# Performance work log

Hardware: AMD Instinct MI355X
Metric: run time of the kernel (lower is better)

## Reference

```python
import jax, jax.numpy as jnp
import numpy as np

H = 512  # hidden_size


def setup_inputs() -> dict:
    key = jax.random.key(0)
    k1, k2, k3, k4, k5, k6 = jax.random.split(key, 6)
    B, S = 32, 2048
    output = jax.random.normal(k1, (B, H), dtype=jnp.float32)
    encoder_outputs = jax.random.normal(k2, (B, S, 2 * H), dtype=jnp.float32)
    encoder_mask = jax.random.randint(k3, (B, S), 0, 2, dtype=jnp.int32)
    # nn.Linear(3H, H): weight [H, 3H], bias [H]
    bound = 1.0 / np.sqrt(3 * H)
    W_attn = jax.random.uniform(k4, (H, 3 * H), minval=-bound, maxval=bound, dtype=jnp.float32)
    b_attn = jax.random.uniform(k5, (H,), minval=-bound, maxval=bound, dtype=jnp.float32)
    v = jax.random.normal(k6, (H,), dtype=jnp.float32) * (1.0 / np.sqrt(H))
    return {"output": output, "encoder_outputs": encoder_outputs,
            "encoder_mask": encoder_mask, "W_attn": W_attn, "b_attn": b_attn, "v": v}


def reference(output, encoder_outputs, encoder_mask, W_attn, b_attn, v):
    # Equivalent to cat([repeat(output), enc], -1) @ W.T: split W into state/enc blocks
    W_s = W_attn[:, :H]        # [H, H]   acts on decoder state
    W_e = W_attn[:, H:]        # [H, 2H]  acts on encoder outputs
    state_proj = output @ W_s.T                              # [B, H]
    enc_proj = jnp.einsum('bse,he->bsh', encoder_outputs, W_e)  # [B, S, H]
    energy = jnp.tanh(state_proj[:, None, :] + enc_proj + b_attn)  # [B, S, H]
    scores = jnp.einsum('bsh,h->bs', energy, v)[:, None, :]   # [B, 1, S]
    scores = scores - 1000.0 * (encoder_mask[:, None, :] == 0).astype(scores.dtype)
    return jax.nn.softmax(scores, axis=2)
```

## Files before the change

### kernel.cpp

```cpp
#include <hip/hip_runtime.h>
#include <hip/hip_bf16.h>

typedef __attribute__((ext_vector_type(4))) float f32x4;
typedef __attribute__((ext_vector_type(8))) short short8;

#define HH 512
#define BB 32
#define SS 2048
#define KK 1024

__device__ __forceinline__ unsigned short f2bf(float f) {
    unsigned int u = __float_as_uint(f);
    u += 0x7fffu + ((u >> 16) & 1u);
    return (unsigned short)(u >> 16);
}

__device__ __forceinline__ ushort4 pack4(float4 f) {
    ushort4 p;
    p.x = f2bf(f.x); p.y = f2bf(f.y); p.z = f2bf(f.z); p.w = f2bf(f.w);
    return p;
}

__device__ __forceinline__ float fast_tanh(float x) {
    float e = __expf(2.0f * x);
    return 1.0f - 2.0f / (e + 1.0f);
}

__device__ __forceinline__ void async_copy16(const void* g, void* l) {
    __builtin_amdgcn_global_load_lds(
        (__attribute__((address_space(1))) const void*)g,
        (__attribute__((address_space(3))) void*)l, 16, 0, 0);
}

__global__ __launch_bounds__(256)
void spb_kernel(const float* __restrict__ out_state,
                const float* __restrict__ W,
                const float* __restrict__ bias,
                float* __restrict__ spb) {
    int wave = threadIdx.x >> 6, lane = threadIdx.x & 63;
    int g = blockIdx.x * 4 + wave;
    int b = g >> 9, h = g & 511;
    const float* wr = W + (size_t)h * 1536;
    const float* ov = out_state + b * HH;
    float4 w0 = *(const float4*)(wr + lane * 8);
    float4 w1 = *(const float4*)(wr + lane * 8 + 4);
    float4 o0 = *(const float4*)(ov + lane * 8);
    float4 o1 = *(const float4*)(ov + lane * 8 + 4);
    float d = w0.x * o0.x + w0.y * o0.y + w0.z * o0.z + w0.w * o0.w
            + w1.x * o1.x + w1.y * o1.y + w1.z * o1.z + w1.w * o1.w;
    d += __shfl_xor(d, 1); d += __shfl_xor(d, 2); d += __shfl_xor(d, 4);
    d += __shfl_xor(d, 8); d += __shfl_xor(d, 16); d += __shfl_xor(d, 32);
    if (lane == 0) spb[g] = d + bias[h];
}

__global__ void wconv_kernel(const float* __restrict__ W, unsigned short* __restrict__ Wt) {
    int idx = blockIdx.x * 256 + threadIdx.x;
    int e8 = idx * 8;
    int h = e8 >> 10;
    int k = e8 & 1023;
    const float* src = W + (size_t)h * 1536 + 512 + k;
    float4 w0 = *(const float4*)src;
    float4 w1 = *(const float4*)(src + 4);
    int kt = k >> 5;
    int q  = (k >> 3) & 3;
    int g  = h >> 4;
    int r  = h & 15;
    int ln = (q << 4) | r;
    unsigned short* dst = Wt + (size_t)kt * 16384 + g * 512 + ln * 8;
    *(ushort4*)dst = pack4(w0);
    *(ushort4*)(dst + 4) = pack4(w1);
}

__global__ __launch_bounds__(512, 4)
void attn_gemm(const float* __restrict__ enc, const unsigned short* __restrict__ Wt,
               const float* __restrict__ spb, const float* __restrict__ vvec,
               float* __restrict__ scores) {
    __shared__ __align__(16) unsigned short Asm[2][2048];
    __shared__ __align__(16) unsigned short Bsm[2][16384];
    __shared__ float red[8][64];

    const int tid = threadIdx.x;
    const int w = tid >> 6;
    const int lane = tid & 63;
    const int r = lane & 15;
    const int q = lane >> 4;
    const int b = blockIdx.x >> 5;
    const int s0 = (blockIdx.x & 31) << 6;

    const int arow = tid >> 3;
    const int akq  = tid & 7;
    const float* asrc = enc + ((size_t)(b * SS + s0 + arow)) * KK + akq * 4;
    const int akey = (arow ^ (arow >> 2)) & 3;
    const int ast  = arow * 32 + ((((akq >> 1) ^ akey) << 3) | ((akq & 1) << 2));

    const unsigned short* bsrc = Wt + tid * 8;

    const int rkey = (r ^ (r >> 2)) & 3;
    const int ard  = r * 32 + ((q ^ rkey) << 3);
    const int brd  = (w * 4) * 512 + lane * 8;

    f32x4 acc[4][4] = {};

    {
        float4 f0 = *(const float4*)asrc;
        #pragma unroll
        for (int c = 0; c < 4; ++c)
            async_copy16(bsrc + c * 4096, &Bsm[0][c * 4096 + tid * 8]);
        *(ushort4*)&Asm[0][ast] = pack4(f0);
    }
    __syncthreads();

    for (int p = 0; p < 32; ++p) {
        const int buf = p & 1;
        float4 f;
        if (p < 31) {
            f = *(const float4*)(asrc + (p + 1) * 32);
            const unsigned short* src = bsrc + (size_t)(p + 1) * 16384;
            #pragma unroll
            for (int c = 0; c < 4; ++c)
                async_copy16(src + c * 4096, &Bsm[buf ^ 1][c * 4096 + tid * 8]);
        }
        short8 af[4], bf[4];
        #pragma unroll
        for (int mt = 0; mt < 4; ++mt)
            af[mt] = *(const short8*)&Asm[buf][mt * 512 + ard];
        #pragma unroll
        for (int nf = 0; nf < 4; ++nf)
            bf[nf] = *(const short8*)&Bsm[buf][nf * 512 + brd];
        #pragma unroll
        for (int mt = 0; mt < 4; ++mt)
            #pragma unroll
            for (int nf = 0; nf < 4; ++nf)
                acc[mt][nf] = __builtin_amdgcn_mfma_f32_16x16x32_bf16(
                    af[mt], bf[nf], acc[mt][nf], 0, 0, 0);
        if (p < 31)
            *(ushort4*)&Asm[buf ^ 1][ast] = pack4(f);
        __syncthreads();
    }

    float vh[4], sh[4];
    #pragma unroll
    for (int nf = 0; nf < 4; ++nf) {
        int h = w * 64 + nf * 16 + r;
        vh[nf] = vvec[h];
        sh[nf] = spb[b * HH + h];
    }
    float rowacc[4][4] = {};
    #pragma unroll
    for (int mt = 0; mt < 4; ++mt)
        #pragma unroll
        for (int nf = 0; nf < 4; ++nf)
            #pragma unroll
            for (int i = 0; i < 4; ++i) {
                float x = acc[mt][nf][i] + sh[nf];
                rowacc[mt][i] += vh[nf] * fast_tanh(x);
            }
    #pragma unroll
    for (int mt = 0; mt < 4; ++mt)
        #pragma unroll
        for (int i = 0; i < 4; ++i) {
            float t = rowacc[mt][i];
            t += __shfl_xor(t, 1);
            t += __shfl_xor(t, 2);
            t += __shfl_xor(t, 4);
            t += __shfl_xor(t, 8);
            rowacc[mt][i] = t;
        }
    if (r == 0) {
        #pragma unroll
        for (int mt = 0; mt < 4; ++mt)
            #pragma unroll
            for (int i = 0; i < 4; ++i)
                red[w][mt * 16 + q * 4 + i] = rowacc[mt][i];
    }
    __syncthreads();
    if (tid < 64) {
        float sum = 0.f;
        #pragma unroll
        for (int ww = 0; ww < 8; ++ww) sum += red[ww][tid];
        scores[b * SS + s0 + tid] = sum;
    }
}

__global__ void softmax_kernel(const float* __restrict__ scores,
                               const int* __restrict__ mask,
                               float* __restrict__ out) {
    __shared__ float red[256];
    int b = blockIdx.x, tid = threadIdx.x;
    float x[8];
    #pragma unroll
    for (int i = 0; i < 8; ++i) {
        int s = tid + i * 256;
        float sc = scores[b * SS + s];
        if (mask[b * SS + s] == 0) sc -= 1000.0f;
        x[i] = sc;
    }
    float mx = x[0];
    #pragma unroll
    for (int i = 1; i < 8; ++i) mx = fmaxf(mx, x[i]);
    red[tid] = mx;
    __syncthreads();
    for (int o = 128; o > 0; o >>= 1) {
        if (tid < o) red[tid] = fmaxf(red[tid], red[tid + o]);
        __syncthreads();
    }
    mx = red[0];
    __syncthreads();
    float e[8], sum = 0.f;
    #pragma unroll
    for (int i = 0; i < 8; ++i) { e[i] = __expf(x[i] - mx); sum += e[i]; }
    red[tid] = sum;
    __syncthreads();
    for (int o = 128; o > 0; o >>= 1) {
        if (tid < o) red[tid] += red[tid + o];
        __syncthreads();
    }
    float inv = 1.0f / red[0];
    #pragma unroll
    for (int i = 0; i < 8; ++i) out[b * SS + tid + i * 256] = e[i] * inv;
}

extern "C" void kernel_launch(void* const* d_in, const int* in_sizes, int n_in,
                              void* d_out, int out_size, void* d_ws, size_t ws_size,
                              hipStream_t stream) {
    const float* out_state = (const float*)d_in[0];
    const float* enc       = (const float*)d_in[1];
    const int*   mask      = (const int*)d_in[2];
    const float* W_attn    = (const float*)d_in[3];
    const float* b_attn    = (const float*)d_in[4];
    const float* vvec      = (const float*)d_in[5];
    float* out = (float*)d_out;

    char* ws = (char*)d_ws;
    float*          spb    = (float*)ws;
    unsigned short* Wt     = (unsigned short*)(ws + 65536);
    float*          scores = (float*)(ws + 65536 + 1048576);

    spb_kernel<<<4096, 256, 0, stream>>>(out_state, W_attn, b_attn, spb);
    wconv_kernel<<<256, 256, 0, stream>>>(W_attn, Wt);
    attn_gemm<<<1024, 512, 0, stream>>>(enc, Wt, spb, vvec, scores);
    softmax_kernel<<<32, 256, 0, stream>>>(scores, mask, out);
}
```

Measured before the change: 445.6 us.

## Deepen A-tile prefetch and use explicit waitcnt barriers in attention GEMM

The encoder-tile global load is now issued two K-steps ahead and held in a register, so it stays in flight across a barrier. The plain __syncthreads is replaced by an explicit s_waitcnt vmcnt(1) plus s_barrier, which waits only for the LDS async copies and leaves the newest load pending. The last two iterations are peeled out of the loop. Each block also rotates the order of its weight-chunk copies by block index, to spread simultaneous accesses across memory channels. The aim is to hide global-memory latency in a loop that looks latency-bound. The cost is more register pressure and hand-written wait counts that depend on the compiler keeping the memory-op order.

```diff
diff --git a/kernel.cpp b/kernel.cpp
--- a/kernel.cpp
+++ b/kernel.cpp
@@ -84,8 +84,9 @@
     const int lane = tid & 63;
     const int r = lane & 15;
     const int q = lane >> 4;
-    const int b = blockIdx.x >> 5;
-    const int s0 = (blockIdx.x & 31) << 6;
+    const int bx = blockIdx.x;
+    const int b = bx >> 5;
+    const int s0 = (bx & 31) << 6;
 
     const int arow = tid >> 3;
     const int akq  = tid & 7;
@@ -101,25 +102,31 @@
 
     f32x4 acc[4][4] = {};
 
-    {
-        float4 f0 = *(const float4*)asrc;
-        #pragma unroll
-        for (int c = 0; c < 4; ++c)
-            async_copy16(bsrc + c * 4096, &Bsm[0][c * 4096 + tid * 8]);
-        *(ushort4*)&Asm[0][ast] = pack4(f0);
-    }
-    __syncthreads();
-
-    for (int p = 0; p < 32; ++p) {
+    #pragma unroll
+    for (int c = 0; c < 4; ++c) {
+        int cc = (c + bx) & 3;
+        async_copy16(bsrc + cc * 4096, &Bsm[0][cc * 4096 + tid * 8]);
+    }
+    asm volatile("" ::: "memory");
+    float4 f0 = *(const float4*)asrc;
+    float4 fcur = *(const float4*)(asrc + 32);
+    asm volatile("" ::: "memory");
+    *(ushort4*)&Asm[0][ast] = pack4(f0);
+    asm volatile("s_waitcnt vmcnt(1) lgkmcnt(0)" ::: "memory");
+    __builtin_amdgcn_s_barrier();
+
+    for (int p = 0; p < 30; ++p) {
         const int buf = p & 1;
-        float4 f;
-        if (p < 31) {
-            f = *(const float4*)(asrc + (p + 1) * 32);
-            const unsigned short* src = bsrc + (size_t)(p + 1) * 16384;
-            #pragma unroll
-            for (int c = 0; c < 4; ++c)
-                async_copy16(src + c * 4096, &Bsm[buf ^ 1][c * 4096 + tid * 8]);
+        #pragma unroll
+        for (int c = 0; c < 4; ++c) {
+            int cc = (c + bx) & 3;
+            async_copy16(bsrc + (size_t)(p + 1) * 16384 + cc * 4096,
+                         &Bsm[buf ^ 1][cc * 4096 + tid * 8]);
         }
+        asm volatile("" ::: "memory");
+        float4 fnext = *(const float4*)(asrc + (size_t)(p + 2) * 32);
+        asm volatile("" ::: "memory");
+
         short8 af[4], bf[4];
         #pragma unroll
         for (int mt = 0; mt < 4; ++mt)
@@ -133,9 +140,53 @@
             for (int nf = 0; nf < 4; ++nf)
                 acc[mt][nf] = __builtin_amdgcn_mfma_f32_16x16x32_bf16(
                     af[mt], bf[nf], acc[mt][nf], 0, 0, 0);
-        if (p < 31)
-            *(ushort4*)&Asm[buf ^ 1][ast] = pack4(f);
-        __syncthreads();
+
+        *(ushort4*)&Asm[buf ^ 1][ast] = pack4(fcur);
+        asm volatile("s_waitcnt vmcnt(1) lgkmcnt(0)" ::: "memory");
+        __builtin_amdgcn_s_barrier();
+        fcur = fnext;
+    }
+
+    {
+        #pragma unroll
+        for (int c = 0; c < 4; ++c) {
+            int cc = (c + bx) & 3;
+            async_copy16(bsrc + (size_t)31 * 16384 + cc * 4096,
+                         &Bsm[1][cc * 4096 + tid * 8]);
+        }
+        asm volatile("" ::: "memory");
+        short8 af[4], bf[4];
+        #pragma unroll
+        for (int mt = 0; mt < 4; ++mt)
+            af[mt] = *(const short8*)&Asm[0][mt * 512 + ard];
+        #pragma unroll
+        for (int nf = 0; nf < 4; ++nf)
+            bf[nf] = *(const short8*)&Bsm[0][nf * 512 + brd];
+        #pragma unroll
+        for (int mt = 0; mt < 4; ++mt)
+            #pragma unroll
+            for (int nf = 0; nf < 4; ++nf)
+                acc[mt][nf] = __builtin_amdgcn_mfma_f32_16x16x32_bf16(
+                    af[mt], bf[nf], acc[mt][nf], 0, 0, 0);
+        *(ushort4*)&Asm[1][ast] = pack4(fcur);
+        asm volatile("s_waitcnt vmcnt(0) lgkmcnt(0)" ::: "memory");
+        __builtin_amdgcn_s_barrier();
+    }
+
+    {
+        short8 af[4], bf[4];
+        #pragma unroll
+        for (int mt = 0; mt < 4; ++mt)
+            af[mt] = *(const short8*)&Asm[1][mt * 512 + ard];
+        #pragma unroll
+        for (int nf = 0; nf < 4; ++nf)
+            bf[nf] = *(const short8*)&Bsm[1][nf * 512 + brd];
+        #pragma unroll
+        for (int mt = 0; mt < 4; ++mt)
+            #pragma unroll
+            for (int nf = 0; nf < 4; ++nf)
+                acc[mt][nf] = __builtin_amdgcn_mfma_f32_16x16x32_bf16(
+                    af[mt], bf[nf], acc[mt][nf], 0, 0, 0);
     }
 
     float vh[4], sh[4];
```

New measurement: 432.1 us. -3.0%, faster.

## Stream fp32 encoder tiles via LDS DMA, convert in-register, read B fragments from global

Applied to the files above, without the earlier changes.

Restructures the attention GEMM so each block covers 128 sequence rows instead of 64. Encoder tiles are copied to LDS as fp32 via global_load_lds with an XOR swizzle and converted to bf16 in registers just before the MFMA. Weight fragments now load straight from global memory into registers, double-buffered, instead of being staged through LDS. Hand-placed waitcnt and barriers pipeline a 128-wide K chunk per stage. This is meant to cut VGPR-staged conversion stores and B-tile LDS traffic and to reuse B across more rows, at the cost of lower occupancy (2 blocks per SM) and 128KB of LDS, plus repeated conversion work.

```diff
diff --git a/kernel.cpp b/kernel.cpp
--- a/kernel.cpp
+++ b/kernel.cpp
@@ -26,10 +26,25 @@
     return 1.0f - 2.0f / (e + 1.0f);
 }
 
-__device__ __forceinline__ void async_copy16(const void* g, void* l) {
+__device__ __forceinline__ void dma16(const float* g, float* l) {
     __builtin_amdgcn_global_load_lds(
         (__attribute__((address_space(1))) const void*)g,
         (__attribute__((address_space(3))) void*)l, 16, 0, 0);
+}
+
+#define FENCE() asm volatile("" ::: "memory")
+
+__device__ __forceinline__ short8 cvt_bf8(f32x4 a0, f32x4 a1) {
+    short8 o;
+    #pragma unroll
+    for (int i = 0; i < 4; ++i) {
+        union { __hip_bfloat16 h; unsigned short u; } c0, c1;
+        c0.h = __float2bfloat16(a0[i]);
+        c1.h = __float2bfloat16(a1[i]);
+        o[i]     = (short)c0.u;
+        o[i + 4] = (short)c1.u;
+    }
+    return o;
 }
 
 __global__ __launch_bounds__(256)
@@ -71,73 +86,122 @@
     *(ushort4*)(dst + 4) = pack4(w1);
 }
 
-__global__ __launch_bounds__(512, 4)
+__global__ __launch_bounds__(512, 2)
 void attn_gemm(const float* __restrict__ enc, const unsigned short* __restrict__ Wt,
                const float* __restrict__ spb, const float* __restrict__ vvec,
                float* __restrict__ scores) {
-    __shared__ __align__(16) unsigned short Asm[2][2048];
-    __shared__ __align__(16) unsigned short Bsm[2][16384];
-    __shared__ float red[8][64];
+    __shared__ __align__(16) float Asm[2][16384];
 
     const int tid = threadIdx.x;
     const int w = tid >> 6;
     const int lane = tid & 63;
     const int r = lane & 15;
     const int q = lane >> 4;
-    const int b = blockIdx.x >> 5;
-    const int s0 = (blockIdx.x & 31) << 6;
-
-    const int arow = tid >> 3;
-    const int akq  = tid & 7;
-    const float* asrc = enc + ((size_t)(b * SS + s0 + arow)) * KK + akq * 4;
-    const int akey = (arow ^ (arow >> 2)) & 3;
-    const int ast  = arow * 32 + ((((akq >> 1) ^ akey) << 3) | ((akq & 1) << 2));
-
-    const unsigned short* bsrc = Wt + tid * 8;
-
-    const int rkey = (r ^ (r >> 2)) & 3;
-    const int ard  = r * 32 + ((q ^ rkey) << 3);
-    const int brd  = (w * 4) * 512 + lane * 8;
-
-    f32x4 acc[4][4] = {};
+    const int b = blockIdx.x >> 4;
+    const int s0 = (blockIdx.x & 15) << 7;
+    const int bS = b * SS + s0;
+
+    const int l32 = lane & 31, lhi = lane >> 5;
+    const int rowA = w * 4 + lhi;
+    const int rowB = w * 4 + 2 + lhi;
+    const float* aP0 = enc + (size_t)(bS + rowA) * KK + ((l32 ^ (rowA & 7)) << 2);
+    const float* aP1 = enc + (size_t)(bS + rowB) * KK + ((l32 ^ (rowB & 7)) << 2);
+    const int ad0 = (w * 4) * 128 + lane * 4;
+    const int ad1 = (w * 4 + 2) * 128 + lane * 4;
+
+    const short8* wp = (const short8*)(Wt + (size_t)(w * 4) * 512 + lane * 8);
+
+    const int ark = r & 7;
+    const int qb = q * 2;
+    const int arf = r * 128;
+
+    f32x4 acc[8][4] = {};
+    short8 bfr[2][4];
+
+    #pragma unroll
+    for (int s = 0; s < 4; ++s) {
+        dma16(aP0 + (size_t)s * 32 * KK, &Asm[0][s * 32 * 128 + ad0]);
+        dma16(aP1 + (size_t)s * 32 * KK, &Asm[0][s * 32 * 128 + ad1]);
+    }
+    FENCE();
+    #pragma unroll
+    for (int nf = 0; nf < 4; ++nf) bfr[0][nf] = wp[nf * 64];
+    FENCE();
+    asm volatile("s_waitcnt vmcnt(4) lgkmcnt(0)" ::: "memory");
+    __builtin_amdgcn_s_barrier();
+    __builtin_amdgcn_sched_barrier(0);
+
+    for (int e = 0; e < 7; ++e) {
+        const float* abase = &Asm[e & 1][0];
+        float* sdst = &Asm[(e & 1) ^ 1][0];
+        const size_t koff = (size_t)(e + 1) * 128;
+        #pragma unroll
+        for (int s = 0; s < 4; ++s) {
+            const int ktn = e * 4 + s + 1;
+            if (s < 3) {
+                #pragma unroll
+                for (int nf = 0; nf < 4; ++nf)
+                    bfr[(s + 1) & 1][nf] = wp[(size_t)ktn * 2048 + nf * 64];
+                FENCE();
+                dma16(aP0 + koff + (size_t)s * 32 * KK, sdst + s * 32 * 128 + ad0);
+                dma16(aP1 + koff + (size_t)s * 32 * KK, sdst + s * 32 * 128 + ad1);
+                FENCE();
+            } else {
+                dma16(aP0 + koff + (size_t)3 * 32 * KK, sdst + 3 * 32 * 128 + ad0);
+                dma16(aP1 + koff + (size_t)3 * 32 * KK, sdst + 3 * 32 * 128 + ad1);
+                FENCE();
+                #pragma unroll
+                for (int nf = 0; nf < 4; ++nf)
+                    bfr[0][nf] = wp[(size_t)ktn * 2048 + nf * 64];
+                FENCE();
+            }
+            const int u0 = ((s * 8 + qb) ^ ark) << 2;
+            const int u1 = ((s * 8 + qb + 1) ^ ark) << 2;
+            #pragma unroll
+            for (int mt = 0; mt < 8; ++mt) {
+                const int rowf = mt * 2048 + arf;
+                f32x4 a0 = *(const f32x4*)(abase + rowf + u0);
+                f32x4 a1 = *(const f32x4*)(abase + rowf + u1);
+                short8 af = cvt_bf8(a0, a1);
+                #pragma unroll
+                for (int nf = 0; nf < 4; ++nf)
+                    acc[mt][nf] = __builtin_amdgcn_mfma_f32_16x16x32_bf16(
+                        af, bfr[s & 1][nf], acc[mt][nf], 0, 0, 0);
+            }
+        }
+        asm volatile("s_waitcnt vmcnt(4) lgkmcnt(0)" ::: "memory");
+        __builtin_amdgcn_s_barrier();
+        __builtin_amdgcn_sched_barrier(0);
+    }
 
     {
-        float4 f0 = *(const float4*)asrc;
-        #pragma unroll
-        for (int c = 0; c < 4; ++c)
-            async_copy16(bsrc + c * 4096, &Bsm[0][c * 4096 + tid * 8]);
-        *(ushort4*)&Asm[0][ast] = pack4(f0);
-    }
-    __syncthreads();
-
-    for (int p = 0; p < 32; ++p) {
-        const int buf = p & 1;
-        float4 f;
-        if (p < 31) {
-            f = *(const float4*)(asrc + (p + 1) * 32);
-            const unsigned short* src = bsrc + (size_t)(p + 1) * 16384;
+        const float* abase = &Asm[1][0];
+        #pragma unroll
+        for (int s = 0; s < 4; ++s) {
+            if (s < 3) {
+                const int ktn = 29 + s;
+                #pragma unroll
+                for (int nf = 0; nf < 4; ++nf)
+                    bfr[(s + 1) & 1][nf] = wp[(size_t)ktn * 2048 + nf * 64];
+                FENCE();
+            }
+            const int u0 = ((s * 8 + qb) ^ ark) << 2;
+            const int u1 = ((s * 8 + qb + 1) ^ ark) << 2;
             #pragma unroll
-            for (int c = 0; c < 4; ++c)
-                async_copy16(src + c * 4096, &Bsm[buf ^ 1][c * 4096 + tid * 8]);
+            for (int mt = 0; mt < 8; ++mt) {
+                const int rowf = mt * 2048 + arf;
+                f32x4 a0 = *(const f32x4*)(abase + rowf + u0);
+                f32x4 a1 = *(const f32x4*)(abase + rowf + u1);
+                short8 af = cvt_bf8(a0, a1);
+                #pragma unroll
+                for (int nf = 0; nf < 4; ++nf)
+                    acc[mt][nf] = __builtin_amdgcn_mfma_f32_16x16x32_bf16(
+                        af, bfr[s & 1][nf], acc[mt][nf], 0, 0, 0);
+            }
         }
-        short8 af[4], bf[4];
-        #pragma unroll
-        for (int mt = 0; mt < 4; ++mt)
-            af[mt] = *(const short8*)&Asm[buf][mt * 512 + ard];
-        #pragma unroll
-        for (int nf = 0; nf < 4; ++nf)
-            bf[nf] = *(const short8*)&Bsm[buf][nf * 512 + brd];
-        #pragma unroll
-        for (int mt = 0; mt < 4; ++mt)
-            #pragma unroll
-            for (int nf = 0; nf < 4; ++nf)
-                acc[mt][nf] = __builtin_amdgcn_mfma_f32_16x16x32_bf16(
-                    af[mt], bf[nf], acc[mt][nf], 0, 0, 0);
-        if (p < 31)
-            *(ushort4*)&Asm[buf ^ 1][ast] = pack4(f);
-        __syncthreads();
-    }
-
+    }
+
+    float* red = (float*)&Asm[0][0];
     float vh[4], sh[4];
     #pragma unroll
     for (int nf = 0; nf < 4; ++nf) {
@@ -145,9 +209,9 @@
         vh[nf] = vvec[h];
         sh[nf] = spb[b * HH + h];
     }
-    float rowacc[4][4] = {};
-    #pragma unroll
-    for (int mt = 0; mt < 4; ++mt)
+    float rowacc[8][4] = {};
+    #pragma unroll
+    for (int mt = 0; mt < 8; ++mt)
         #pragma unroll
         for (int nf = 0; nf < 4; ++nf)
             #pragma unroll
@@ -156,7 +220,7 @@
                 rowacc[mt][i] += vh[nf] * fast_tanh(x);
             }
     #pragma unroll
-    for (int mt = 0; mt < 4; ++mt)
+    for (int mt = 0; mt < 8; ++mt)
         #pragma unroll
         for (int i = 0; i < 4; ++i) {
             float t = rowacc[mt][i];
@@ -168,17 +232,17 @@
         }
     if (r == 0) {
         #pragma unroll
-        for (int mt = 0; mt < 4; ++mt)
+        for (int mt = 0; mt < 8; ++mt)
             #pragma unroll
             for (int i = 0; i < 4; ++i)
-                red[w][mt * 16 + q * 4 + i] = rowacc[mt][i];
+                red[w * 128 + mt * 16 + q * 4 + i] = rowacc[mt][i];
     }
     __syncthreads();
-    if (tid < 64) {
+    if (tid < 128) {
         float sum = 0.f;
         #pragma unroll
-        for (int ww = 0; ww < 8; ++ww) sum += red[ww][tid];
-        scores[b * SS + s0 + tid] = sum;
+        for (int ww = 0; ww < 8; ++ww) sum += red[ww * 128 + tid];
+        scores[bS + tid] = sum;
     }
 }
 
@@ -238,6 +302,6 @@
 
     spb_kernel<<<4096, 256, 0, stream>>>(out_state, W_attn, b_attn, spb);
     wconv_kernel<<<256, 256, 0, stream>>>(W_attn, Wt);
-    attn_gemm<<<1024, 512, 0, stream>>>(enc, Wt, spb, vvec, scores);
+    attn_gemm<<<512, 512, 0, stream>>>(enc, Wt, spb, vvec, scores);
     softmax_kernel<<<32, 256, 0, stream>>>(scores, mask, out);
 }
```

New measurement: 413.1 us. -7.3%, faster.
